# Kernel tuning notes

Hardware: AMD Instinct MI355X
Metric: run time of the kernel (lower is better)

## Reference

```python
import jax, jax.numpy as jnp
import numpy as np
from jax import lax

V = 5001   # vocab_size = len(word2id)+1
E = 128    # embedding_dim
H = 256    # hidden_dim
HH = H // 2  # per-direction hidden
T = 9      # tag_len
B, S = 256, 512


def setup_inputs() -> dict:
    key = jax.random.key(0)
    ks = jax.random.split(key, 16)
    sc = 0.08
    n = lambda k, shp: (jax.random.normal(k, shp) * sc).astype(jnp.float32)
    return {
        "x": jax.random.randint(ks[0], (B, S), 0, V),
        "mask": jnp.ones((B, S), jnp.float32),
        "embed_table": n(ks[1], (V, E)),
        "Wih_f": n(ks[2], (4 * HH, E)), "Whh_f": n(ks[3], (4 * HH, HH)),
        "bih_f": n(ks[4], (4 * HH,)), "bhh_f": n(ks[5], (4 * HH,)),
        "Wih_b": n(ks[6], (4 * HH, E)), "Whh_b": n(ks[7], (4 * HH, HH)),
        "bih_b": n(ks[8], (4 * HH,)), "bhh_b": n(ks[9], (4 * HH,)),
        "W_out": n(ks[10], (T, H)), "b_out": n(ks[11], (T,)),
        "transitions": n(ks[12], (T, T)),
        "start_trans": n(ks[13], (T,)),
        "end_trans": n(ks[14], (T,)),
    }


def _lstm_dir(xs, Wih, Whh, bih, bhh, reverse):
    # xs: [S,B,E]; torch gate order i,f,g,o
    Bx = xs.shape[1]
    h0 = jnp.zeros((Bx, HH), xs.dtype)
    pre_x = jnp.einsum('sbe,ge->sbg', xs, Wih) + bih + bhh  # hoist input proj

    def step(carry, px):
        h, c = carry
        g = px + h @ Whh.T
        i, f, gg, o = jnp.split(g, 4, axis=-1)
        c = jax.nn.sigmoid(f) * c + jax.nn.sigmoid(i) * jnp.tanh(gg)
        h = jax.nn.sigmoid(o) * jnp.tanh(c)
        return (h, c), h

    _, hs = lax.scan(step, (h0, h0), pre_x, reverse=reverse)
    return hs  # [S,B,HH]


def _viterbi(emissions, mask, transitions, start_trans, end_trans):
    # emissions: [B,S,T], mask: [B,S] bool -> tags [B,S] int32, best score [B]
    Bx = emissions.shape[0]
    em_t = emissions.transpose(1, 0, 2)        # [S,B,T]
    score0 = start_trans + em_t[0]             # [B,T]
    idT = jnp.arange(T, dtype=jnp.int32)

    def step(score, inp):
        em, m = inp                            # em [B,T], m [B]
        cand = score[:, :, None] + transitions[None]     # [B,Tprev,Tcur]
        best = jnp.max(cand, axis=1) + em
        bp = jnp.argmax(cand, axis=1).astype(jnp.int32)  # [B,T]
        new_score = jnp.where(m[:, None], best, score)
        bp = jnp.where(m[:, None], bp, idT[None, :])
        return new_score, bp

    score, bps = lax.scan(step, score0, (em_t[1:], mask.T[1:]))  # bps [S-1,B,T]
    score = score + end_trans
    best_score = jnp.max(score, axis=-1)                          # [B]
    last = jnp.argmax(score, axis=-1).astype(jnp.int32)           # [B]

    def back(tag, bp_t):
        prev = jnp.take_along_axis(bp_t, tag[:, None], axis=1)[:, 0]
        return prev, prev

    _, prevs = lax.scan(back, last, bps, reverse=True)            # [S-1,B]
    tags = jnp.concatenate([prevs, last[None, :]], axis=0).T      # [B,S]
    return tags, best_score


def reference(x, mask, embed_table, Wih_f, Whh_f, bih_f, bhh_f,
              Wih_b, Whh_b, bih_b, bhh_b, W_out, b_out,
              transitions, start_trans, end_trans):
    emb = embed_table[x]                       # [B,S,E]
    xs = emb.transpose(1, 0, 2)                # [S,B,E]
    hf = _lstm_dir(xs, Wih_f, Whh_f, bih_f, bhh_f, reverse=False)
    hb = _lstm_dir(xs, Wih_b, Whh_b, bih_b, bhh_b, reverse=True)
    hs = jnp.concatenate([hf, hb], axis=-1).transpose(1, 0, 2)   # [B,S,H]
    # dropout is identity at inference
    em = hs @ W_out.T + b_out                  # [B,S,T]
    em = em * mask[..., None]
    tags, best_score = _viterbi(em, mask > 0, transitions, start_trans, end_trans)
    return tags, best_score
```

## Files before the change

kernel.cpp:

```cpp
#include <hip/hip_runtime.h>
#include <hip/hip_bf16.h>
#include <math.h>

#define S_LEN 512
#define B_SZ  256
#define E_DIM 128
#define HHID  128
#define G4    512
#define T_TAG 9
#define NR    (S_LEN * B_SZ)
#define VOCAB 5001

typedef __attribute__((ext_vector_type(8))) short bf16x8;
typedef __attribute__((ext_vector_type(4))) float f32x4;

__device__ __forceinline__ float bf2f(__hip_bfloat16 v) { return __bfloat162float(v); }
__device__ __forceinline__ float scrub0(float v) {
    unsigned u = __float_as_uint(v);
    return (((u >> 23) & 0xFFu) == 0xFFu) ? 0.f : v;
}
__device__ __forceinline__ float frcp(float x) { return __builtin_amdgcn_rcpf(x); }
__device__ __forceinline__ float fsig(float x) { return frcp(1.f + __expf(-x)); }
__device__ __forceinline__ float ftanh(float x) {
    return 1.f - 2.f * frcp(1.f + __expf(2.f * x));
}

__device__ __hip_bfloat16 g_emb[VOCAB * E_DIM];
__device__ __hip_bfloat16 g_wih[2][G4 * E_DIM];
__device__ __hip_bfloat16 g_whh2[2][G4 * HHID];
__device__ __align__(16) float g_bias[2][G4];
__device__ float g_wout[T_TAG * 256];
__device__ float g_bout[T_TAG];
__device__ float g_trans[T_TAG * T_TAG];
__device__ float g_start[T_TAG];
__device__ float g_end[T_TAG];
__device__ float g_maskf[B_SZ * S_LEN];
__device__ float g_em[(long)NR * T_TAG];
__device__ __align__(16) float g_hs[2][(long)NR * HHID];
__device__ __align__(16) float g_px[(long)2 * S_LEN * 16 * 128 * 16 * 4];

__global__ __launch_bounds__(256) void fill_out(float* out, int n) {
    const int i = blockIdx.x * 256 + threadIdx.x;
    if (i < n) out[i] = 0.f;
}

__global__ __launch_bounds__(256) void convert_kernel(
    const void* mask, const void* emb,
    const void* wih_f, const void* whh_f, const void* bih_f, const void* bhh_f,
    const void* wih_b, const void* whh_b, const void* bih_b, const void* bhh_b,
    const void* wout, const void* bout, const void* trans,
    const void* startt, const void* endt)
{
    const bool isb = (((const unsigned*)mask)[0] == 0x3F803F80u);
    auto ldf = [&](const void* p, long i) -> float {
        float v = isb ? bf2f(((const __hip_bfloat16*)p)[i]) : ((const float*)p)[i];
        return scrub0(v);
    };
    const long tid0   = (long)blockIdx.x * blockDim.x + threadIdx.x;
    const long stride = (long)gridDim.x * blockDim.x;

    for (long i = tid0; i < (long)VOCAB * E_DIM; i += stride)
        g_emb[i] = __float2bfloat16(ldf(emb, i));
    for (long i = tid0; i < (long)G4 * E_DIM; i += stride) {
        const int np = (int)(i >> 7), e = (int)(i & 127);
        const int g = np & 3, u = np >> 2;
        const long src = (long)(g * 128 + u) * E_DIM + e;
        g_wih[0][i] = __float2bfloat16(ldf(wih_f, src));
        g_wih[1][i] = __float2bfloat16(ldf(wih_b, src));
    }
    for (long i = tid0; i < (long)G4 * HHID; i += stride) {
        const int np = (int)(i >> 7), k = (int)(i & 127);
        const int g = np & 3, u = np >> 2;
        const long src = (long)(g * 128 + u) * HHID + k;
        g_whh2[0][i] = __float2bfloat16(ldf(whh_f, src));
        g_whh2[1][i] = __float2bfloat16(ldf(whh_b, src));
    }
    for (long i = tid0; i < G4; i += stride) {
        const int g = (int)i & 3, u = (int)i >> 2;
        const long src = g * 128 + u;
        g_bias[0][i] = ldf(bih_f, src) + ldf(bhh_f, src);
        g_bias[1][i] = ldf(bih_b, src) + ldf(bhh_b, src);
    }
    for (long i = tid0; i < T_TAG * 256; i += stride) g_wout[i] = ldf(wout, i);
    for (long i = tid0; i < T_TAG * T_TAG; i += stride) g_trans[i] = ldf(trans, i);
    for (long i = tid0; i < T_TAG; i += stride) {
        g_bout[i]  = ldf(bout, i);
        g_start[i] = ldf(startt, i);
        g_end[i]   = ldf(endt, i);
    }
    for (long i = tid0; i < (long)B_SZ * S_LEN; i += stride)
        g_maskf[i] = ldf(mask, i);
}

__global__ __launch_bounds__(512, 2) void px_gemm(const int* __restrict__ x)
{
    const int bg = blockIdx.x, dir = blockIdx.y, sc = blockIdx.z;
    const int tid  = threadIdx.x;
    const int lane = tid & 63, wv = tid >> 6;
    const int m16  = lane & 15, quad = lane >> 4;

    bf16x8 V[4][4];
    f32x4 bias4[4];
    #pragma unroll
    for (int t = 0; t < 4; t++) {
        const int np = (wv * 4 + t) * 16 + m16;
        #pragma unroll
        for (int kk = 0; kk < 4; kk++)
            V[t][kk] = *(const bf16x8*)&g_wih[dir][(long)np * E_DIM + kk * 32 + quad * 8];
        const int u = 16 * wv + 4 * t + quad;
        const float4 b4 = *(const float4*)&g_bias[dir][4 * u];
        bias4[t] = (f32x4){b4.x, b4.y, b4.z, b4.w};
    }
    const bool x64 = ((x[1] | x[3] | x[5] | x[7]) == 0);
    const int b = bg * 16 + m16;
    const int s0 = sc * 64;
    for (int s = s0; s < s0 + 64; s++) {
        const int ii = b * S_LEN + s;
        const int xo = (x64 ? x[2 * ii] : x[ii]) * E_DIM;
        bf16x8 E[4];
        #pragma unroll
        for (int kk = 0; kk < 4; kk++)
            E[kk] = *(const bf16x8*)&g_emb[(long)xo + kk * 32 + quad * 8];
        #pragma unroll
        for (int t = 0; t < 4; t++) {
            f32x4 px = bias4[t];
            #pragma unroll
            for (int kk = 0; kk < 4; kk++)
                px = __builtin_amdgcn_mfma_f32_16x16x32_bf16(V[t][kk], E[kk], px, 0, 0, 0);
            const int u = 16 * wv + 4 * t + quad;
            const long idx = (((long)(dir * S_LEN + s) * 16 + bg) * 128 + u) * 64 + m16 * 4;
            *(f32x4*)&g_px[idx] = px;
        }
    }
}

#define SCAN_STEP(RD, PX)                                                      \
  {                                                                            \
    const int wr_ = (RD) ^ 1;                                                  \
    bf16x8 Hh_[4], Hl_[4];                                                     \
    _Pragma("unroll")                                                          \
    for (int kk = 0; kk < 4; kk++) {                                           \
        const int off_ = ((kk * 4 + quad) * 16 + m16) * 8;                     \
        Hh_[kk] = *(const bf16x8*)&hB[RD][0][off_];                            \
        Hl_[kk] = *(const bf16x8*)&hB[RD][1][off_];                            \
    }                                                                          \
    _Pragma("unroll")                                                          \
    for (int t = 0; t < 4; t++) {                                              \
        _Pragma("unroll")                                                      \
        for (int kk = 0; kk < 4; kk++) {                                       \
            PX[t] = __builtin_amdgcn_mfma_f32_16x16x32_bf16(W[t][kk], Hh_[kk], PX[t], 0, 0, 0); \
            PX[t] = __builtin_amdgcn_mfma_f32_16x16x32_bf16(W[t][kk], Hl_[kk], PX[t], 0, 0, 0); \
        }                                                                      \
    }                                                                          \
    _Pragma("unroll")                                                          \
    for (int t = 0; t < 4; t++) {                                              \
        const float iv = fsig(PX[t][0]);                                       \
        const float fv = fsig(PX[t][1]);                                       \
        const float gv = ftanh(PX[t][2]);                                      \
        const float ov = fsig(PX[t][3]);                                       \
        c[t] = fv * c[t] + iv * gv;                                            \
        const float h = ov * ftanh(c[t]);                                      \
        const int u = 16 * wv + 4 * t + quad;                                  \
        const unsigned ub = __float_as_uint(h);                                \
        const unsigned hb_ = ub >> 16;                                         \
        const float hif = __uint_as_float(ub & 0xFFFF0000u);                   \
        const unsigned lb_ = __float_as_uint(h - hif) >> 16;                   \
        const int ha = (u >> 3) * 128 + m16 * 8 + (u & 7);                     \
        hB[wr_][0][ha] = (unsigned short)hb_;                                  \
        hB[wr_][1][ha] = (unsigned short)lb_;                                  \
        hsp[t * 64] = h;                                                       \
    }                                                                          \
    {            \
        const float* pf_ = (itv + 2 < S_LEN) ? (pxp + 2 * pxd) : pxp;          \
        PX[0] = *(const f32x4*)(pf_ + 0);                                      \
        PX[1] = *(const f32x4*)(pf_ + 256);                                    \
        PX[2] = *(const f32x4*)(pf_ + 512);                                    \
        PX[3] = *(const f32x4*)(pf_ + 768);                                    \
    }                                                                          \
    asm volatile("s_waitcnt lgkmcnt(0)" ::: "memory");                         \
    __builtin_amdgcn_sched_barrier(0);                                         \
    __builtin_amdgcn_s_barrier();                                              \
    __builtin_amdgcn_sched_barrier(0);                                         \
    hsp += hsd; pxp += pxd; itv++;                                             \
  }

__global__ __launch_bounds__(512, 2) void scan_mfma()
{
    __shared__ __align__(16) unsigned short hB[2][2][16 * 16 * 8];

    const int bg = blockIdx.x, dir = blockIdx.y;
    const int tid  = threadIdx.x;
    const int lane = tid & 63, wv = tid >> 6;
    const int m16  = lane & 15, quad = lane >> 4;

    bf16x8 W[4][4];
    #pragma unroll
    for (int t = 0; t < 4; t++) {
        const int np = (wv * 4 + t) * 16 + m16;
        #pragma unroll
        for (int kk = 0; kk < 4; kk++)
            W[t][kk] = *(const bf16x8*)&g_whh2[dir][(long)np * HHID + kk * 32 + quad * 8];
    }
    for (int i = tid; i < 2 * 2 * 2048; i += 512) ((unsigned short*)hB)[i] = 0;
    float c[4] = {0.f, 0.f, 0.f, 0.f};

    const int se0  = dir ? (S_LEN - 1) : 0;
    const int step = dir ? -1 : 1;
    const int u0   = 16 * wv + quad;

    const float* pxp = &g_px[(((long)(dir * S_LEN + se0) * 16 + bg) * 128 + u0) * 64 + m16 * 4];
    const long pxd = (long)step * 131072;

    f32x4 pxA[4], pxB[4];
    #pragma unroll
    for (int t = 0; t < 4; t++) pxA[t] = *(const f32x4*)(pxp + t * 256);
    {
        const float* p1 = pxp + pxd;
        #pragma unroll
        for (int t = 0; t < 4; t++) pxB[t] = *(const f32x4*)(p1 + t * 256);
    }

    float* hsp = &g_hs[dir][((long)(se0 * 16 + bg) * 128 + u0) * 16 + m16];
    const long hsd = (long)step * 32768;

    int itv = 0;
    __syncthreads();

    for (int it = 0; it < S_LEN; it += 2) {
        SCAN_STEP(0, pxA)
        SCAN_STEP(1, pxB)
    }
}

__global__ __launch_bounds__(256, 4) void emission_kernel()
{
    __shared__ float hfL[2048], hbL[2048];
    __shared__ float Wsh[T_TAG][256];
    __shared__ float bo[T_TAG];
    const int tid = threadIdx.x, blk = blockIdx.x;
    for (int i = tid; i < T_TAG * 256; i += 256) Wsh[i >> 8][i & 255] = g_wout[i];
    if (tid < T_TAG) bo[tid] = g_bout[tid];
    const float* hf = &g_hs[0][(long)blk * 2048];
    const float* hb = &g_hs[1][(long)blk * 2048];
    for (int i = tid; i < 2048; i += 256) { hfL[i] = hf[i]; hbL[i] = hb[i]; }
    __syncthreads();

    const int m = tid & 15, j = tid >> 4;
    if (j < T_TAG) {
        float acc = bo[j];
        #pragma unroll 4
        for (int u = 0; u < 128; u++)
            acc += hfL[u * 16 + m] * Wsh[j][u] + hbL[u * 16 + m] * Wsh[j][128 + u];
        const int r = (blk >> 4) * 256 + (blk & 15) * 16 + m;
        g_em[(long)r * T_TAG + j] = scrub0(acc);
    }
}

__global__ __launch_bounds__(256, 2)
void viterbi_kernel(float* __restrict__ out, int out_size)
{
    __shared__ unsigned char bp[4][S_LEN][T_TAG];
    const int wid  = threadIdx.x >> 6;
    const int lane = threadIdx.x & 63;
    const int b  = blockIdx.x * 4 + wid;
    const int jj = (lane < T_TAG) ? lane : 0;

    float tcol[T_TAG];
    #pragma unroll
    for (int i = 0; i < T_TAG; i++) tcol[i] = g_trans[i * T_TAG + jj];

    float score[T_TAG];
    {
        const float m0 = g_maskf[b * S_LEN + 0];
        #pragma unroll
        for (int i = 0; i < T_TAG; i++)
            score[i] = g_start[i] + g_em[(long)b * T_TAG + i] * m0;
    }
    float e = g_em[((long)1 * B_SZ + b) * T_TAG + jj];
    float m = g_maskf[b * S_LEN + 1];

    for (int s = 1; s < S_LEN; s++) {
        float en = 0.f, mn = 0.f;
        if (s + 1 < S_LEN) {
            en = g_em[((long)(s + 1) * B_SZ + b) * T_TAG + jj];
            mn = g_maskf[b * S_LEN + s + 1];
        }
        float best = score[0] + tcol[0];
        int arg = 0;
        #pragma unroll
        for (int i = 1; i < T_TAG; i++) {
            const float cnd = score[i] + tcol[i];
            if (cnd > best) { best = cnd; arg = i; }
        }
        float ns; int nbp;
        if (m > 0.f) { ns = best + e * m; nbp = arg; }
        else         { ns = score[jj];    nbp = jj;  }
        if (lane < T_TAG) bp[wid][s][jj] = (unsigned char)nbp;
        #pragma unroll
        for (int i = 0; i < T_TAG; i++) score[i] = __shfl(ns, i, 64);
        e = en; m = mn;
    }
    #pragma unroll
    for (int i = 0; i < T_TAG; i++) score[i] += g_end[i];

    __syncthreads();

    if (lane == 0) {
        float bs = score[0]; int last = 0;
        #pragma unroll
        for (int i = 1; i < T_TAG; i++)
            if (score[i] > bs) { bs = score[i]; last = i; }
        {
            const unsigned u = __float_as_uint(bs);
            if (((u >> 23) & 0xFFu) == 0xFFu) bs = -100.f;
        }
        if ((long)B_SZ * S_LEN + b < out_size)
            out[(long)B_SZ * S_LEN + b] = bs;
        int tag = last;
        if (tag < 0) tag = 0; if (tag > 8) tag = 8;
        out[(long)b * S_LEN + (S_LEN - 1)] = (float)tag;
        for (int s2 = S_LEN - 1; s2 >= 1; s2--) {
            tag = bp[wid][s2][tag];
            if (tag < 0) tag = 0; if (tag > 8) tag = 8;
            out[(long)b * S_LEN + (s2 - 1)] = (float)tag;
        }
    }
}

extern "C" void kernel_launch(void* const* d_in, const int* in_sizes, int n_in,
                              void* d_out, int out_size, void* d_ws, size_t ws_size,
                              hipStream_t stream) {
    const int* x = (const int*)d_in[0];
    float* out = (float*)d_out;

    fill_out<<<(out_size + 255) / 256, 256, 0, stream>>>(out, out_size);
    convert_kernel<<<512, 256, 0, stream>>>(
        d_in[1], d_in[2], d_in[3], d_in[4], d_in[5], d_in[6],
        d_in[7], d_in[8], d_in[9], d_in[10], d_in[11], d_in[12],
        d_in[13], d_in[14], d_in[15]);
    px_gemm<<<dim3(16, 2, 8), 512, 0, stream>>>(x);
    scan_mfma<<<dim3(16, 2), 512, 0, stream>>>();
    emission_kernel<<<8192, 256, 0, stream>>>();
    viterbi_kernel<<<64, 256, 0, stream>>>(out, out_size);
}
```

Measured before the change: 988.9 us.

## Precompute input projection per vocabulary entry and gather it in the scan

Replaces the per-token input-projection GEMM over all B*S tokens with a GEMM over the 5001 vocabulary rows, producing a per-token projection table. The scan kernel now stages token offsets in shared memory and gathers the precomputed gate preactivations by token id. This drops roughly 256MB of px writes and reads and most of the projection FLOPs. In exchange the scan does data-dependent gather loads, which are less coalesced and could stall the latency-bound recurrence.

```diff
diff --git a/kernel.cpp b/kernel.cpp
--- a/kernel.cpp
+++ b/kernel.cpp
@@ -10,6 +10,7 @@
 #define T_TAG 9
 #define NR    (S_LEN * B_SZ)
 #define VOCAB 5001
+#define VOCABP 5008
 
 typedef __attribute__((ext_vector_type(8))) short bf16x8;
 typedef __attribute__((ext_vector_type(4))) float f32x4;
@@ -37,7 +38,7 @@
 __device__ float g_maskf[B_SZ * S_LEN];
 __device__ float g_em[(long)NR * T_TAG];
 __device__ __align__(16) float g_hs[2][(long)NR * HHID];
-__device__ __align__(16) float g_px[(long)2 * S_LEN * 16 * 128 * 16 * 4];
+__device__ __align__(16) float g_pxv[(long)2 * VOCABP * 128 * 4];
 
 __global__ __launch_bounds__(256) void fill_out(float* out, int n) {
     const int i = blockIdx.x * 256 + threadIdx.x;
@@ -92,9 +93,9 @@
         g_maskf[i] = ldf(mask, i);
 }
 
-__global__ __launch_bounds__(512, 2) void px_gemm(const int* __restrict__ x)
-{
-    const int bg = blockIdx.x, dir = blockIdx.y, sc = blockIdx.z;
+__global__ __launch_bounds__(512, 2) void pxv_gemm()
+{
+    const int grp = blockIdx.x, dir = blockIdx.y;
     const int tid  = threadIdx.x;
     const int lane = tid & 63, wv = tid >> 6;
     const int m16  = lane & 15, quad = lane >> 4;
@@ -111,26 +112,21 @@
         const float4 b4 = *(const float4*)&g_bias[dir][4 * u];
         bias4[t] = (f32x4){b4.x, b4.y, b4.z, b4.w};
     }
-    const bool x64 = ((x[1] | x[3] | x[5] | x[7]) == 0);
-    const int b = bg * 16 + m16;
-    const int s0 = sc * 64;
-    for (int s = s0; s < s0 + 64; s++) {
-        const int ii = b * S_LEN + s;
-        const int xo = (x64 ? x[2 * ii] : x[ii]) * E_DIM;
-        bf16x8 E[4];
+    const int v  = grp * 16 + m16;
+    const int vv = (v < VOCAB) ? v : 0;
+    bf16x8 E[4];
+    #pragma unroll
+    for (int kk = 0; kk < 4; kk++)
+        E[kk] = *(const bf16x8*)&g_emb[(long)vv * E_DIM + kk * 32 + quad * 8];
+    #pragma unroll
+    for (int t = 0; t < 4; t++) {
+        f32x4 px = bias4[t];
         #pragma unroll
         for (int kk = 0; kk < 4; kk++)
-            E[kk] = *(const bf16x8*)&g_emb[(long)xo + kk * 32 + quad * 8];
-        #pragma unroll
-        for (int t = 0; t < 4; t++) {
-            f32x4 px = bias4[t];
-            #pragma unroll
-            for (int kk = 0; kk < 4; kk++)
-                px = __builtin_amdgcn_mfma_f32_16x16x32_bf16(V[t][kk], E[kk], px, 0, 0, 0);
-            const int u = 16 * wv + 4 * t + quad;
-            const long idx = (((long)(dir * S_LEN + s) * 16 + bg) * 128 + u) * 64 + m16 * 4;
-            *(f32x4*)&g_px[idx] = px;
-        }
+            px = __builtin_amdgcn_mfma_f32_16x16x32_bf16(V[t][kk], E[kk], px, 0, 0, 0);
+        const int u = 16 * wv + 4 * t + quad;
+        if (v < VOCAB)
+            *(f32x4*)&g_pxv[((long)(dir * VOCABP + v) * 128 + u) * 4] = px;
     }
 }
 
@@ -170,23 +166,27 @@
         hB[wr_][1][ha] = (unsigned short)lb_;                                  \
         hsp[t * 64] = h;                                                       \
     }                                                                          \
-    {            \
-        const float* pf_ = (itv + 2 < S_LEN) ? (pxp + 2 * pxd) : pxp;          \
+    {       \
+        int se2 = sev + 2 * step;                                              \
+        se2 = se2 < 0 ? 0 : (se2 > S_LEN - 1 ? S_LEN - 1 : se2);               \
+        const int off2 = xO[se2 * 16 + m16];                                   \
+        const float* pf_ = pxvL + off2;                                        \
         PX[0] = *(const f32x4*)(pf_ + 0);                                      \
-        PX[1] = *(const f32x4*)(pf_ + 256);                                    \
-        PX[2] = *(const f32x4*)(pf_ + 512);                                    \
-        PX[3] = *(const f32x4*)(pf_ + 768);                                    \
+        PX[1] = *(const f32x4*)(pf_ + 16);                                     \
+        PX[2] = *(const f32x4*)(pf_ + 32);                                     \
+        PX[3] = *(const f32x4*)(pf_ + 48);                                     \
     }                                                                          \
     asm volatile("s_waitcnt lgkmcnt(0)" ::: "memory");                         \
     __builtin_amdgcn_sched_barrier(0);                                         \
     __builtin_amdgcn_s_barrier();                                              \
     __builtin_amdgcn_sched_barrier(0);                                         \
-    hsp += hsd; pxp += pxd; itv++;                                             \
+    hsp += hsd; sev += step; itv++;                                            \
   }
 
-__global__ __launch_bounds__(512, 2) void scan_mfma()
+__global__ __launch_bounds__(512, 2) void scan_mfma(const int* __restrict__ x)
 {
     __shared__ __align__(16) unsigned short hB[2][2][16 * 16 * 8];
+    __shared__ int xO[S_LEN * 16];
 
     const int bg = blockIdx.x, dir = blockIdx.y;
     const int tid  = threadIdx.x;
@@ -201,30 +201,41 @@
         for (int kk = 0; kk < 4; kk++)
             W[t][kk] = *(const bf16x8*)&g_whh2[dir][(long)np * HHID + kk * 32 + quad * 8];
     }
+    {
+        const bool x64 = ((x[1] | x[3] | x[5] | x[7]) == 0);
+        for (int i = tid; i < S_LEN * 16; i += 512) {
+            const int s = i >> 4, m = i & 15;
+            const int ii = (bg * 16 + m) * S_LEN + s;
+            int tok = x64 ? x[2 * ii] : x[ii];
+            tok = (unsigned)tok < VOCAB ? tok : 0;
+            xO[i] = tok * 512;
+        }
+    }
     for (int i = tid; i < 2 * 2 * 2048; i += 512) ((unsigned short*)hB)[i] = 0;
     float c[4] = {0.f, 0.f, 0.f, 0.f};
+    __syncthreads();
 
     const int se0  = dir ? (S_LEN - 1) : 0;
     const int step = dir ? -1 : 1;
     const int u0   = 16 * wv + quad;
 
-    const float* pxp = &g_px[(((long)(dir * S_LEN + se0) * 16 + bg) * 128 + u0) * 64 + m16 * 4];
-    const long pxd = (long)step * 131072;
+    const float* pxvL = &g_pxv[(long)dir * VOCABP * 512 + u0 * 4];
 
     f32x4 pxA[4], pxB[4];
-    #pragma unroll
-    for (int t = 0; t < 4; t++) pxA[t] = *(const f32x4*)(pxp + t * 256);
     {
-        const float* p1 = pxp + pxd;
-        #pragma unroll
-        for (int t = 0; t < 4; t++) pxB[t] = *(const f32x4*)(p1 + t * 256);
+        const int o0 = xO[se0 * 16 + m16];
+        #pragma unroll
+        for (int t = 0; t < 4; t++) pxA[t] = *(const f32x4*)(pxvL + o0 + 16 * t);
+        const int se1 = (S_LEN > 1) ? se0 + step : se0;
+        const int o1 = xO[se1 * 16 + m16];
+        #pragma unroll
+        for (int t = 0; t < 4; t++) pxB[t] = *(const f32x4*)(pxvL + o1 + 16 * t);
     }
 
     float* hsp = &g_hs[dir][((long)(se0 * 16 + bg) * 128 + u0) * 16 + m16];
     const long hsd = (long)step * 32768;
 
-    int itv = 0;
-    __syncthreads();
+    int itv = 0, sev = se0;
 
     for (int it = 0; it < S_LEN; it += 2) {
         SCAN_STEP(0, pxA)
@@ -338,8 +349,8 @@
         d_in[1], d_in[2], d_in[3], d_in[4], d_in[5], d_in[6],
         d_in[7], d_in[8], d_in[9], d_in[10], d_in[11], d_in[12],
         d_in[13], d_in[14], d_in[15]);
-    px_gemm<<<dim3(16, 2, 8), 512, 0, stream>>>(x);
-    scan_mfma<<<dim3(16, 2), 512, 0, stream>>>();
+    pxv_gemm<<<dim3((VOCABP / 16), 2), 512, 0, stream>>>();
+    scan_mfma<<<dim3(16, 2), 512, 0, stream>>>(x);
     emission_kernel<<<8192, 256, 0, stream>>>();
     viterbi_kernel<<<64, 256, 0, stream>>>(out, out_size);
 }
```

Result: faster. 938.3 us (-5.1%).
